# Kernel tuning notes

Measured on AMD Instinct MI355X. Metric: run time of the kernel, lower is better.

Reference implementation:

```python
import jax, jax.numpy as jnp
import numpy as np

N_NODES = 100000
N_EDGES = 600000
N_FEAT = 128
N_HID = 128
N_GRAPHS = 256


def gcn_conv(x, src, dst, W, b, n_nodes):
    # PyG GCNConv: h = x @ W; add self-loops; sym-normalize; scatter-add; + bias
    h = x @ W  # [N, H]
    loop = jnp.arange(n_nodes)
    s = jnp.concatenate([src, loop])
    d = jnp.concatenate([dst, loop])
    deg = jax.ops.segment_sum(jnp.ones_like(d, dtype=h.dtype), d, num_segments=n_nodes)
    dinv = jnp.where(deg > 0, jax.lax.rsqrt(deg), 0.0)
    norm = dinv[s] * dinv[d]  # [E+N]
    msg = h[s] * norm[:, None]  # gather + scale
    out = jax.ops.segment_sum(msg, d, num_segments=n_nodes)  # scatter-add
    return out + b


def setup_inputs() -> dict:
    key = jax.random.key(0)
    ks = jax.random.split(key, 12)
    x = jax.random.normal(ks[0], (N_NODES, N_FEAT), dtype=jnp.float32)
    edge_index = jax.random.randint(ks[1], (2, N_EDGES), 0, N_NODES, dtype=jnp.int64)
    batch = jnp.sort(jax.random.randint(ks[2], (N_NODES,), 0, N_GRAPHS, dtype=jnp.int64))
    def lin(k, fi, fo):
        s = 1.0 / np.sqrt(fi)
        return jax.random.uniform(k, (fi, fo), jnp.float32, -s, s)
    params = {
        'W1': lin(ks[3], N_FEAT, N_HID), 'b1': jnp.zeros((N_HID,), jnp.float32),
        'W2': lin(ks[4], N_HID, N_HID), 'b2': jnp.zeros((N_HID,), jnp.float32),
        'W3': lin(ks[5], N_HID, N_HID), 'b3': jnp.zeros((N_HID,), jnp.float32),
        'W4': lin(ks[6], N_HID, N_HID), 'b4': jnp.zeros((N_HID,), jnp.float32),
        'Ws1': lin(ks[7], N_HID, N_HID), 'bs1': jnp.zeros((N_HID,), jnp.float32),
        'Ws2': lin(ks[8], N_HID, 1), 'bs2': jnp.zeros((1,), jnp.float32),
    }
    return {'x': x, 'edge_index': edge_index, 'batch': batch, **params}


def reference(x, edge_index, batch, W1, b1, W2, b2, W3, b3, W4, b4, Ws1, bs1, Ws2, bs2):
    src, dst = edge_index[0], edge_index[1]
    h = x
    # 2 conv blocks = 4 GCNConv layers, each followed by ReLU
    for W, b in ((W1, b1), (W2, b2), (W3, b3), (W4, b4)):
        h = jax.nn.relu(gcn_conv(h, src, dst, W, b, N_NODES))
    # global mean pool over nodes per graph
    sums = jax.ops.segment_sum(h, batch, num_segments=N_GRAPHS)  # [G, H]
    cnt = jax.ops.segment_sum(jnp.ones((h.shape[0],), h.dtype), batch, num_segments=N_GRAPHS)
    pooled = sums / jnp.maximum(cnt, 1.0)[:, None]
    # summary MLP: Linear -> ReLU -> Linear(->1)
    out = jax.nn.relu(pooled @ Ws1 + bs1) @ Ws2 + bs2  # [G, 1]
    return out
```

## Files before the change

### kernel.cpp

```cpp
#include <hip/hip_runtime.h>

#define N_NODES 100000
#define N_EDGES 600000
#define NF 128
#define NG 256

typedef _Float16 f16;
typedef f16 half8 __attribute__((ext_vector_type(8)));
typedef f16 half4v __attribute__((ext_vector_type(4)));
typedef float float4v __attribute__((ext_vector_type(4)));


__global__ void k_count(const int* __restrict__ ei, int* __restrict__ counts) {
    int e = blockIdx.x * 256 + threadIdx.x;
    if (e < N_EDGES) atomicAdd(&counts[ei[N_EDGES + e]], 1);
}

__global__ void k_scan1(const int* __restrict__ counts, int* __restrict__ row_ptr,
                        int* __restrict__ bsums, float* __restrict__ dinv) {
    __shared__ int s[256];
    int b = blockIdx.x, t = threadIdx.x;
    int base = b * 2048 + t * 8;
    int local[8];
    int sum = 0;
#pragma unroll
    for (int q = 0; q < 8; q++) {
        int idx = base + q;
        int v = (idx < N_NODES) ? counts[idx] : 0;
        if (idx < N_NODES) dinv[idx] = 1.0f / sqrtf((float)(v + 1));
        local[q] = sum;
        sum += v;
    }
    s[t] = sum;
    __syncthreads();
    for (int off = 1; off < 256; off <<= 1) {
        int v = 0;
        if (t >= off) v = s[t - off];
        __syncthreads();
        s[t] += v;
        __syncthreads();
    }
    int excl = s[t] - sum;
#pragma unroll
    for (int q = 0; q < 8; q++) {
        int idx = base + q;
        if (idx < N_NODES) row_ptr[idx] = excl + local[q];
    }
    if (t == 255) bsums[b] = s[255];
}

__global__ void k_scan3(int* __restrict__ row_ptr, const int* __restrict__ bsums,
                        int* __restrict__ cursor) {
    __shared__ int pre;
    if (threadIdx.x == 0) {
        int g = blockIdx.x >> 3;
        int s = 0;
        for (int j = 0; j < g; j++) s += bsums[j];
        pre = s;
    }
    __syncthreads();
    int i = blockIdx.x * 256 + threadIdx.x;
    if (i < N_NODES) {
        int v = row_ptr[i] + pre;
        row_ptr[i] = v;
        cursor[i] = v;
        if (i == 0) row_ptr[N_NODES] = N_EDGES;
    }
}

__global__ void k_fill(const int* __restrict__ ei, int* __restrict__ cursor,
                       int* __restrict__ col,
                       const float* __restrict__ W1, const float* __restrict__ W2,
                       const float* __restrict__ W3, const float* __restrict__ W4,
                       f16* __restrict__ wtH) {
    int e = blockIdx.x * 256 + threadIdx.x;
    if (e < N_EDGES) {
        int d = ei[N_EDGES + e];
        int p = atomicAdd(&cursor[d], 1);
        col[p] = ei[e];
    }
    if (blockIdx.x < 256) {
        int idx = blockIdx.x * 256 + threadIdx.x;
        int layer = idx >> 14;
        int rem = idx & 16383;
        int j = rem & 7;
        int lane = (rem >> 3) & 63;
        int chunk = rem >> 9;
        int wave = chunk >> 3;
        int s = (chunk >> 1) & 3;
        int ct = chunk & 1;
        int n = wave * 32 + ct * 16 + (lane & 15);
        int k = s * 32 + (lane >> 4) * 8 + j;
        const float* W = (layer == 0) ? W1 : (layer == 1) ? W2 : (layer == 2) ? W3 : W4;
        wtH[layer * 16384 + rem] = (f16)W[k * NF + n];
    }
}


__device__ __forceinline__ void agg_tail(const half8* __restrict__ z8,
                                         const int* __restrict__ col,
                                         int sbase, int fl, int beg, int end,
                                         float acc[8]) {
    for (int c = beg + 16; c < end; c += 16) {
        int ce = c + fl;
        int cv = (ce < end) ? col[ce] : 0;
        int mc = end - c; if (mc > 16) mc = 16;
        for (int j = 0; j < mc; j += 4) {
            int kk = mc - j;
            half8 v0 = {}, v1 = {}, v2 = {}, v3 = {};
            int s0 = __shfl(cv, sbase + j + 0, 64);
            v0 = z8[(size_t)s0 * 16 + fl];
            if (kk > 1) { int s1 = __shfl(cv, sbase + j + 1, 64); v1 = z8[(size_t)s1 * 16 + fl]; }
            if (kk > 2) { int s2 = __shfl(cv, sbase + j + 2, 64); v2 = z8[(size_t)s2 * 16 + fl]; }
            if (kk > 3) { int s3 = __shfl(cv, sbase + j + 3, 64); v3 = z8[(size_t)s3 * 16 + fl]; }
#pragma unroll
            for (int q = 0; q < 8; q++) acc[q] += (float)v0[q];
            if (kk > 1) {
#pragma unroll
                for (int q = 0; q < 8; q++) acc[q] += (float)v1[q];
            }
            if (kk > 2) {
#pragma unroll
                for (int q = 0; q < 8; q++) acc[q] += (float)v2[q];
            }
            if (kk > 3) {
#pragma unroll
                for (int q = 0; q < 8; q++) acc[q] += (float)v3[q];
            }
        }
    }
}

__device__ __forceinline__ void agg_pair(const half8* __restrict__ z8,
                                         const int* __restrict__ col,
                                         int sbase, int fl,
                                         int begA, int endA, int begB, int endB,
                                         int colvA, int colvB,
                                         float accA[8], float accB[8]) {
    int mA = endA - begA; if (mA > 16) mA = 16;
    int mB = endB - begB; if (mB > 16) mB = 16;
    const int mmax = (mA > mB) ? mA : mB;
    for (int j = 0; j < mmax; j += 4) {
        const int kA = mA - j, kB = mB - j;
        half8 vA0 = {}, vA1 = {}, vA2 = {}, vA3 = {};
        half8 vB0 = {}, vB1 = {}, vB2 = {}, vB3 = {};
        if (kA > 0) {
            int s0 = __shfl(colvA, sbase + j + 0, 64);
            vA0 = z8[(size_t)s0 * 16 + fl];
            if (kA > 1) { int s1 = __shfl(colvA, sbase + j + 1, 64); vA1 = z8[(size_t)s1 * 16 + fl]; }
            if (kA > 2) { int s2 = __shfl(colvA, sbase + j + 2, 64); vA2 = z8[(size_t)s2 * 16 + fl]; }
            if (kA > 3) { int s3 = __shfl(colvA, sbase + j + 3, 64); vA3 = z8[(size_t)s3 * 16 + fl]; }
        }
        if (kB > 0) {
            int s0 = __shfl(colvB, sbase + j + 0, 64);
            vB0 = z8[(size_t)s0 * 16 + fl];
            if (kB > 1) { int s1 = __shfl(colvB, sbase + j + 1, 64); vB1 = z8[(size_t)s1 * 16 + fl]; }
            if (kB > 2) { int s2 = __shfl(colvB, sbase + j + 2, 64); vB2 = z8[(size_t)s2 * 16 + fl]; }
            if (kB > 3) { int s3 = __shfl(colvB, sbase + j + 3, 64); vB3 = z8[(size_t)s3 * 16 + fl]; }
        }
        if (kA > 0) {
#pragma unroll
            for (int q = 0; q < 8; q++) accA[q] += (float)vA0[q];
            if (kA > 1) {
#pragma unroll
                for (int q = 0; q < 8; q++) accA[q] += (float)vA1[q];
            }
            if (kA > 2) {
#pragma unroll
                for (int q = 0; q < 8; q++) accA[q] += (float)vA2[q];
            }
            if (kA > 3) {
#pragma unroll
                for (int q = 0; q < 8; q++) accA[q] += (float)vA3[q];
            }
        }
        if (kB > 0) {
#pragma unroll
            for (int q = 0; q < 8; q++) accB[q] += (float)vB0[q];
            if (kB > 1) {
#pragma unroll
                for (int q = 0; q < 8; q++) accB[q] += (float)vB1[q];
            }
            if (kB > 2) {
#pragma unroll
                for (int q = 0; q < 8; q++) accB[q] += (float)vB2[q];
            }
            if (kB > 3) {
#pragma unroll
                for (int q = 0; q < 8; q++) accB[q] += (float)vB3[q];
            }
        }
    }
    if (endA - begA > 16) agg_tail(z8, col, sbase, fl, begA, endA, accA);
    if (endB - begB > 16) agg_tail(z8, col, sbase, fl, begB, endB, accB);
}


__global__ __launch_bounds__(256) void k_gemm1(
    const float* __restrict__ X, const f16* __restrict__ WTH,
    const float* __restrict__ dinv, f16* __restrict__ Z, int M) {
    __shared__ __align__(16) f16 As[64 * 136];
    __shared__ float sdi[64];

    const int t = threadIdx.x;
    const int row0 = blockIdx.x * 64;
    const int wave = t >> 6;
    const int lane = t & 63;
    const int nl = lane & 15;
    const int quad = lane >> 4;

    auto bofs = [&](int s, int ct) {
        return (size_t)((((wave * 8 + s * 2 + ct) * 64) + lane) << 3);
    };

    half8 cbh[2];
    cbh[0] = *(const half8*)(WTH + bofs(0, 0));
    cbh[1] = *(const half8*)(WTH + bofs(0, 1));

    if (t < 64) sdi[t] = (row0 + t < M) ? dinv[row0 + t] : 0.f;
#pragma unroll
    for (int q = 0; q < 8; q++) {
        int lin = t + q * 256;
        int r = lin >> 5, c4 = lin & 31;
        float4 v = make_float4(0.f, 0.f, 0.f, 0.f);
        if (row0 + r < M) v = ((const float4*)(X + (size_t)(row0 + r) * NF))[c4];
        half4v hv = {(f16)v.x, (f16)v.y, (f16)v.z, (f16)v.w};
        *(half4v*)&As[r * 136 + c4 * 4] = hv;
    }
    __syncthreads();

    float4v acc[2][4];
#pragma unroll
    for (int ct = 0; ct < 2; ct++)
#pragma unroll
        for (int rt = 0; rt < 4; rt++) acc[ct][rt] = (float4v)0.f;

#pragma unroll
    for (int s = 0; s < 4; s++) {
        half8 nbh[2];
        if (s < 3) {
            nbh[0] = *(const half8*)(WTH + bofs(s + 1, 0));
            nbh[1] = *(const half8*)(WTH + bofs(s + 1, 1));
        }
        half8 fa[4];
#pragma unroll
        for (int rt = 0; rt < 4; rt++)
            fa[rt] = *(half8*)&As[(rt * 16 + nl) * 136 + s * 32 + quad * 8];
#pragma unroll
        for (int ct = 0; ct < 2; ct++)
#pragma unroll
            for (int rt = 0; rt < 4; rt++)
                acc[ct][rt] = __builtin_amdgcn_mfma_f32_16x16x32_f16(fa[rt], cbh[ct], acc[ct][rt], 0, 0, 0);
        if (s < 3) {
            cbh[0] = nbh[0]; cbh[1] = nbh[1];
        }
    }

    __syncthreads();
#pragma unroll
    for (int ct = 0; ct < 2; ct++)
#pragma unroll
        for (int rt = 0; rt < 4; rt++)
#pragma unroll
            for (int r = 0; r < 4; r++)
                As[(rt * 16 + quad * 4 + r) * 136 + wave * 32 + ct * 16 + nl] =
                    (f16)(acc[ct][rt][r] * sdi[rt * 16 + quad * 4 + r]);
    __syncthreads();
#pragma unroll
    for (int q = 0; q < 4; q++) {
        int lin = t + q * 256;
        int r = lin >> 4, c8 = lin & 15;
        if (row0 + r < M)
            *(half8*)(Z + (size_t)(row0 + r) * NF + c8 * 8) = *(half8*)&As[r * 136 + c8 * 8];
    }
}


#define ACHUNK 4

__global__ __launch_bounds__(256) void k_agg_gemm(
    const f16* __restrict__ z, const float* __restrict__ dinv,
    const int* __restrict__ row_ptr, const int* __restrict__ col,
    const float* __restrict__ bias,
    const f16* __restrict__ WTH,
    f16* __restrict__ Zout) {
    __shared__ __align__(16) f16 As[64 * 136];
    __shared__ float sdi[64];

    const int t = threadIdx.x;
    const int slot = t >> 4;
    const int fl = t & 15;
    const int sbase = (t & 48);
    const int n0 = (blockIdx.x * 16 + slot) * ACHUNK;
    const half8* z8 = (const half8*)z;

    float bb[8];
    {
        float4 b0 = ((const float4*)bias)[fl * 2];
        float4 b1 = ((const float4*)bias)[fl * 2 + 1];
        bb[0] = b0.x; bb[1] = b0.y; bb[2] = b0.z; bb[3] = b0.w;
        bb[4] = b1.x; bb[5] = b1.y; bb[6] = b1.z; bb[7] = b1.w;
    }

    int rp[5];
#pragma unroll
    for (int i = 0; i < 5; i++) {
        int n = n0 + i;
        rp[i] = row_ptr[(n < N_NODES) ? n : N_NODES];
    }
    float dis[4]; half8 selfv[4]; int colv0[4];
#pragma unroll
    for (int i = 0; i < 4; i++) {
        int n = n0 + i;
        bool ok = n < N_NODES;
        half8 zz = {};
        dis[i] = ok ? dinv[n] : 0.f;
        selfv[i] = ok ? z8[(size_t)n * 16 + fl] : zz;
        int ce = rp[i] + fl;
        colv0[i] = (ce < rp[i + 1]) ? col[ce] : 0;
    }
    if (fl == 0) {
#pragma unroll
        for (int i = 0; i < 4; i++) sdi[slot * ACHUNK + i] = dis[i];
    }

#pragma unroll
    for (int p = 0; p < 2; p++) {
        const int iA = 2 * p, iB = 2 * p + 1;
        float accA[8], accB[8];
#pragma unroll
        for (int q = 0; q < 8; q++) {
            accA[q] = (float)selfv[iA][q];
            accB[q] = (float)selfv[iB][q];
        }
        agg_pair(z8, col, sbase, fl, rp[iA], rp[iA + 1], rp[iB], rp[iB + 1],
                 colv0[iA], colv0[iB], accA, accB);
        half8 oA, oB;
#pragma unroll
        for (int q = 0; q < 8; q++) {
            oA[q] = (f16)fmaxf(bb[q] + dis[iA] * accA[q], 0.f);
            oB[q] = (f16)fmaxf(bb[q] + dis[iB] * accB[q], 0.f);
        }
        *(half8*)&As[(slot * ACHUNK + iA) * 136 + fl * 8] = oA;
        *(half8*)&As[(slot * ACHUNK + iB) * 136 + fl * 8] = oB;
    }

    const int wave = t >> 6;
    const int lane = t & 63;
    const int nl = lane & 15;
    const int quad = lane >> 4;
    const int row0 = blockIdx.x * 64;

    auto bofs = [&](int s, int ct) {
        return (size_t)((((wave * 8 + s * 2 + ct) * 64) + lane) << 3);
    };

    half8 cbh[2];
    cbh[0] = *(const half8*)(WTH + bofs(0, 0));
    cbh[1] = *(const half8*)(WTH + bofs(0, 1));
    __syncthreads();

    float4v acc[2][4];
#pragma unroll
    for (int ct = 0; ct < 2; ct++)
#pragma unroll
        for (int rt = 0; rt < 4; rt++) acc[ct][rt] = (float4v)0.f;

#pragma unroll
    for (int s = 0; s < 4; s++) {
        half8 nbh[2];
        if (s < 3) {
            nbh[0] = *(const half8*)(WTH + bofs(s + 1, 0));
            nbh[1] = *(const half8*)(WTH + bofs(s + 1, 1));
        }
        half8 fa[4];
#pragma unroll
        for (int rt = 0; rt < 4; rt++)
            fa[rt] = *(half8*)&As[(rt * 16 + nl) * 136 + s * 32 + quad * 8];
#pragma unroll
        for (int ct = 0; ct < 2; ct++)
#pragma unroll
            for (int rt = 0; rt < 4; rt++)
                acc[ct][rt] = __builtin_amdgcn_mfma_f32_16x16x32_f16(fa[rt], cbh[ct], acc[ct][rt], 0, 0, 0);
        if (s < 3) {
            cbh[0] = nbh[0]; cbh[1] = nbh[1];
        }
    }

    __syncthreads();
#pragma unroll
    for (int ct = 0; ct < 2; ct++)
#pragma unroll
        for (int rt = 0; rt < 4; rt++)
#pragma unroll
            for (int r = 0; r < 4; r++)
                As[(rt * 16 + quad * 4 + r) * 136 + wave * 32 + ct * 16 + nl] =
                    (f16)(acc[ct][rt][r] * sdi[rt * 16 + quad * 4 + r]);
    __syncthreads();
#pragma unroll
    for (int q = 0; q < 4; q++) {
        int lin = t + q * 256;
        int r = lin >> 4, c8 = lin & 15;
        if (row0 + r < N_NODES)
            *(half8*)(Zout + (size_t)(row0 + r) * NF + c8 * 8) = *(half8*)&As[r * 136 + c8 * 8];
    }
}


#define HP 132

__global__ __launch_bounds__(256) void k_agg_pool(
    const f16* __restrict__ z, const float* __restrict__ dinv,
    const int* __restrict__ row_ptr, const int* __restrict__ col,
    const float* __restrict__ bias, const int* __restrict__ batch,
    float* __restrict__ pooled) {
    __shared__ float hs[64 * HP];
    __shared__ int gids[64];

    const int t = threadIdx.x;
    const int slot = t >> 4;
    const int fl = t & 15;
    const int sbase = (t & 48);
    const int n0 = (blockIdx.x * 16 + slot) * ACHUNK;
    const int base_node = blockIdx.x * 64;
    const half8* z8 = (const half8*)z;

    float bb[8];
    {
        float4 b0 = ((const float4*)bias)[fl * 2];
        float4 b1 = ((const float4*)bias)[fl * 2 + 1];
        bb[0] = b0.x; bb[1] = b0.y; bb[2] = b0.z; bb[3] = b0.w;
        bb[4] = b1.x; bb[5] = b1.y; bb[6] = b1.z; bb[7] = b1.w;
    }

    if (t < 64) {
        int n = base_node + t;
        gids[t] = (n < N_NODES) ? batch[n] : -1;
    }

    int rp[5];
#pragma unroll
    for (int i = 0; i < 5; i++) {
        int n = n0 + i;
        rp[i] = row_ptr[(n < N_NODES) ? n : N_NODES];
    }
    float dis[4]; half8 selfv[4]; int colv0[4];
#pragma unroll
    for (int i = 0; i < 4; i++) {
        int n = n0 + i;
        bool ok = n < N_NODES;
        half8 zz = {};
        dis[i] = ok ? dinv[n] : 0.f;
        selfv[i] = ok ? z8[(size_t)n * 16 + fl] : zz;
        int ce = rp[i] + fl;
        colv0[i] = (ce < rp[i + 1]) ? col[ce] : 0;
    }

#pragma unroll
    for (int p = 0; p < 2; p++) {
        const int iA = 2 * p, iB = 2 * p + 1;
        float accA[8], accB[8];
#pragma unroll
        for (int q = 0; q < 8; q++) {
            accA[q] = (float)selfv[iA][q];
            accB[q] = (float)selfv[iB][q];
        }
        agg_pair(z8, col, sbase, fl, rp[iA], rp[iA + 1], rp[iB], rp[iB + 1],
                 colv0[iA], colv0[iB], accA, accB);
        float4v a0, a1, b0v, b1v;
#pragma unroll
        for (int q = 0; q < 4; q++) {
            a0[q]  = fmaxf(bb[q]     + dis[iA] * accA[q],     0.f);
            a1[q]  = fmaxf(bb[q + 4] + dis[iA] * accA[q + 4], 0.f);
            b0v[q] = fmaxf(bb[q]     + dis[iB] * accB[q],     0.f);
            b1v[q] = fmaxf(bb[q + 4] + dis[iB] * accB[q + 4], 0.f);
        }
        *(float4v*)&hs[(slot * ACHUNK + iA) * HP + fl * 8]     = a0;
        *(float4v*)&hs[(slot * ACHUNK + iA) * HP + fl * 8 + 4] = a1;
        *(float4v*)&hs[(slot * ACHUNK + iB) * HP + fl * 8]     = b0v;
        *(float4v*)&hs[(slot * ACHUNK + iB) * HP + fl * 8 + 4] = b1v;
    }
    __syncthreads();

    if (t < NF) {
        float acc = 0.f;
        int curg = -1;
        for (int r = 0; r < 64; r++) {
            int g = gids[r];
            if (g < 0) break;
            if (g != curg) {
                if (curg >= 0) atomicAdd(&pooled[curg * NF + t], acc);
                acc = 0.f;
                curg = g;
            }
            acc += hs[r * HP + t];
        }
        if (curg >= 0) atomicAdd(&pooled[curg * NF + t], acc);
    }
}


__global__ void k_mlp(const float* __restrict__ pooled, const int* __restrict__ batch,
                      const float* __restrict__ Ws1, const float* __restrict__ bs1,
                      const float* __restrict__ Ws2, const float* __restrict__ bs2,
                      float* __restrict__ out) {
    __shared__ float row[NF];
    __shared__ float red[NF];
    int g = blockIdx.x, f = threadIdx.x;
    int lo = 0, hi = N_NODES;
    while (lo < hi) { int mid = (lo + hi) >> 1; if (batch[mid] < g) lo = mid + 1; else hi = mid; }
    int start = lo;
    hi = N_NODES;
    while (lo < hi) { int mid = (lo + hi) >> 1; if (batch[mid] < g + 1) lo = mid + 1; else hi = mid; }
    float cnt = (float)(lo - start);
    row[f] = pooled[g * NF + f] / fmaxf(cnt, 1.f);
    __syncthreads();
    float t = bs1[f];
    for (int k = 0; k < NF; k++) t += row[k] * Ws1[k * NF + f];
    t = fmaxf(t, 0.f);
    red[f] = t * Ws2[f];
    __syncthreads();
    for (int s = 64; s > 0; s >>= 1) {
        if (f < s) red[f] += red[f + s];
        __syncthreads();
    }
    if (f == 0) out[g] = red[0] + bs2[0];
}


extern "C" void kernel_launch(void* const* d_in, const int* in_sizes, int n_in,
                              void* d_out, int out_size, void* d_ws, size_t ws_size,
                              hipStream_t stream) {
    const float* x    = (const float*)d_in[0];
    const int*   ei   = (const int*)d_in[1];
    const int*   batch= (const int*)d_in[2];
    const float* W1 = (const float*)d_in[3];  const float* b1 = (const float*)d_in[4];
    const float* W2 = (const float*)d_in[5];  const float* b2 = (const float*)d_in[6];
    const float* W3 = (const float*)d_in[7];  const float* b3 = (const float*)d_in[8];
    const float* W4 = (const float*)d_in[9];  const float* b4 = (const float*)d_in[10];
    const float* Ws1= (const float*)d_in[11]; const float* bs1= (const float*)d_in[12];
    const float* Ws2= (const float*)d_in[13]; const float* bs2= (const float*)d_in[14];
    float* out = (float*)d_out;

    char* ws = (char*)d_ws;
    size_t off = 0;
    auto alloc = [&](size_t bytes) {
        void* p = ws + off;
        off += (bytes + 255) & ~(size_t)255;
        return p;
    };
    f16*   bufA   = (f16*)alloc((size_t)N_NODES * NF * 2);
    f16*   bufB   = (f16*)alloc((size_t)N_NODES * NF * 2);
    f16*   wtH    = (f16*)alloc((size_t)4 * NF * NF * 2);
    int*   counts = (int*)alloc((size_t)N_NODES * 4);
    int*   row_ptr= (int*)alloc((size_t)(N_NODES + 1) * 4);
    int*   cursor = (int*)alloc((size_t)N_NODES * 4);
    int*   col    = (int*)alloc((size_t)N_EDGES * 4);
    int*   bsums  = (int*)alloc(64 * 4);
    float* dinv   = (float*)alloc((size_t)N_NODES * 4);
    float* pooled = (float*)alloc((size_t)NG * NF * 4);

    hipMemsetAsync(counts, 0, (size_t)N_NODES * 4, stream);
    hipMemsetAsync(pooled, 0, (size_t)NG * NF * 4, stream);
    k_count<<<(N_EDGES + 255) / 256, 256, 0, stream>>>(ei, counts);
    int nscan = (N_NODES + 2047) / 2048;
    k_scan1<<<nscan, 256, 0, stream>>>(counts, row_ptr, bsums, dinv);
    k_scan3<<<(N_NODES + 255) / 256, 256, 0, stream>>>(row_ptr, bsums, cursor);
    k_fill<<<(N_EDGES + 255) / 256, 256, 0, stream>>>(ei, cursor, col,
                                                      W1, W2, W3, W4, wtH);

    int gblocks = (N_NODES + 63) / 64;

    k_gemm1<<<gblocks, 256, 0, stream>>>(x, wtH, dinv, bufA, N_NODES);
    k_agg_gemm<<<gblocks, 256, 0, stream>>>(bufA, dinv, row_ptr, col, b1,
                                            wtH + 16384, bufB);
    k_agg_gemm<<<gblocks, 256, 0, stream>>>(bufB, dinv, row_ptr, col, b2,
                                            wtH + 32768, bufA);
    k_agg_gemm<<<gblocks, 256, 0, stream>>>(bufA, dinv, row_ptr, col, b3,
                                            wtH + 49152, bufB);
    k_agg_pool<<<gblocks, 256, 0, stream>>>(bufB, dinv, row_ptr, col, b4,
                                            batch, pooled);
    k_mlp<<<NG, 128, 0, stream>>>(pooled, batch, Ws1, bs1, Ws2, bs2, out);
}
```

Baseline: 361.9 us.

## Fuse preprocessing and epilogue kernels to cut launch count

Replaces the two memsets and the weight conversion with one init kernel. Merges the two-pass scan into a single-pass scan with decoupled lookback over block sums, and runs the CSR fill concurrently with the first GEMM inside one launch. The final MLP moves into the last-finishing block of the pool kernel through an atomic counter. This removes several launches and their serialization gaps, at the cost of a serial MLP over all 256 graphs in one block and spin-waits in the scan.

```diff
diff --git a/kernel.cpp b/kernel.cpp
--- a/kernel.cpp
+++ b/kernel.cpp
@@ -4,97 +4,16 @@
 #define N_EDGES 600000
 #define NF 128
 #define NG 256
+#define GBLK 1563
+#define EBLK 2344
+#define ACHUNK 4
+#define HP 132
+#define SFLAG (1 << 30)
 
 typedef _Float16 f16;
 typedef f16 half8 __attribute__((ext_vector_type(8)));
 typedef f16 half4v __attribute__((ext_vector_type(4)));
 typedef float float4v __attribute__((ext_vector_type(4)));
-
-
-__global__ void k_count(const int* __restrict__ ei, int* __restrict__ counts) {
-    int e = blockIdx.x * 256 + threadIdx.x;
-    if (e < N_EDGES) atomicAdd(&counts[ei[N_EDGES + e]], 1);
-}
-
-__global__ void k_scan1(const int* __restrict__ counts, int* __restrict__ row_ptr,
-                        int* __restrict__ bsums, float* __restrict__ dinv) {
-    __shared__ int s[256];
-    int b = blockIdx.x, t = threadIdx.x;
-    int base = b * 2048 + t * 8;
-    int local[8];
-    int sum = 0;
-#pragma unroll
-    for (int q = 0; q < 8; q++) {
-        int idx = base + q;
-        int v = (idx < N_NODES) ? counts[idx] : 0;
-        if (idx < N_NODES) dinv[idx] = 1.0f / sqrtf((float)(v + 1));
-        local[q] = sum;
-        sum += v;
-    }
-    s[t] = sum;
-    __syncthreads();
-    for (int off = 1; off < 256; off <<= 1) {
-        int v = 0;
-        if (t >= off) v = s[t - off];
-        __syncthreads();
-        s[t] += v;
-        __syncthreads();
-    }
-    int excl = s[t] - sum;
-#pragma unroll
-    for (int q = 0; q < 8; q++) {
-        int idx = base + q;
-        if (idx < N_NODES) row_ptr[idx] = excl + local[q];
-    }
-    if (t == 255) bsums[b] = s[255];
-}
-
-__global__ void k_scan3(int* __restrict__ row_ptr, const int* __restrict__ bsums,
-                        int* __restrict__ cursor) {
-    __shared__ int pre;
-    if (threadIdx.x == 0) {
-        int g = blockIdx.x >> 3;
-        int s = 0;
-        for (int j = 0; j < g; j++) s += bsums[j];
-        pre = s;
-    }
-    __syncthreads();
-    int i = blockIdx.x * 256 + threadIdx.x;
-    if (i < N_NODES) {
-        int v = row_ptr[i] + pre;
-        row_ptr[i] = v;
-        cursor[i] = v;
-        if (i == 0) row_ptr[N_NODES] = N_EDGES;
-    }
-}
-
-__global__ void k_fill(const int* __restrict__ ei, int* __restrict__ cursor,
-                       int* __restrict__ col,
-                       const float* __restrict__ W1, const float* __restrict__ W2,
-                       const float* __restrict__ W3, const float* __restrict__ W4,
-                       f16* __restrict__ wtH) {
-    int e = blockIdx.x * 256 + threadIdx.x;
-    if (e < N_EDGES) {
-        int d = ei[N_EDGES + e];
-        int p = atomicAdd(&cursor[d], 1);
-        col[p] = ei[e];
-    }
-    if (blockIdx.x < 256) {
-        int idx = blockIdx.x * 256 + threadIdx.x;
-        int layer = idx >> 14;
-        int rem = idx & 16383;
-        int j = rem & 7;
-        int lane = (rem >> 3) & 63;
-        int chunk = rem >> 9;
-        int wave = chunk >> 3;
-        int s = (chunk >> 1) & 3;
-        int ct = chunk & 1;
-        int n = wave * 32 + ct * 16 + (lane & 15);
-        int k = s * 32 + (lane >> 4) * 8 + j;
-        const float* W = (layer == 0) ? W1 : (layer == 1) ? W2 : (layer == 2) ? W3 : W4;
-        wtH[layer * 16384 + rem] = (f16)W[k * NF + n];
-    }
-}
 
 
 __device__ __forceinline__ void agg_tail(const half8* __restrict__ z8,
@@ -196,13 +115,116 @@
 }
 
 
-__global__ __launch_bounds__(256) void k_gemm1(
+__global__ void k_init(int* __restrict__ counts, float* __restrict__ pooled,
+                       int* __restrict__ bsums, int* __restrict__ ctrl,
+                       const float* __restrict__ W1, const float* __restrict__ W2,
+                       const float* __restrict__ W3, const float* __restrict__ W4,
+                       f16* __restrict__ wtH) {
+    int gtid = blockIdx.x * 256 + threadIdx.x;
+    int gs = gridDim.x * 256;
+    for (int i = gtid; i < N_NODES; i += gs) counts[i] = 0;
+    for (int i = gtid; i < NG * NF; i += gs) pooled[i] = 0.f;
+    if (gtid < 64) bsums[gtid] = 0;
+    if (gtid >= 64 && gtid < 80) ctrl[gtid - 64] = 0;
+    for (int idx = gtid; idx < 65536; idx += gs) {
+        int layer = idx >> 14;
+        int rem = idx & 16383;
+        int j = rem & 7;
+        int lane = (rem >> 3) & 63;
+        int chunk = rem >> 9;
+        int wave = chunk >> 3;
+        int s = (chunk >> 1) & 3;
+        int ct = chunk & 1;
+        int n = wave * 32 + ct * 16 + (lane & 15);
+        int k = s * 32 + (lane >> 4) * 8 + j;
+        const float* W = (layer == 0) ? W1 : (layer == 1) ? W2 : (layer == 2) ? W3 : W4;
+        wtH[layer * 16384 + rem] = (f16)W[k * NF + n];
+    }
+}
+
+
+__global__ void k_count(const int* __restrict__ ei, int* __restrict__ counts) {
+    int e = blockIdx.x * 256 + threadIdx.x;
+    if (e < N_EDGES) atomicAdd(&counts[ei[N_EDGES + e]], 1);
+}
+
+
+__global__ __launch_bounds__(256) void k_scan(const int* __restrict__ counts,
+                                              int* __restrict__ row_ptr,
+                                              int* __restrict__ cursor,
+                                              int* __restrict__ bsums,
+                                              float* __restrict__ dinv) {
+    __shared__ int s[256];
+    __shared__ int spre;
+    int b = blockIdx.x, t = threadIdx.x;
+    int base = b * 2048 + t * 8;
+    int local[8];
+    int sum = 0;
+#pragma unroll
+    for (int q = 0; q < 8; q++) {
+        int idx = base + q;
+        int v = (idx < N_NODES) ? counts[idx] : 0;
+        if (idx < N_NODES) dinv[idx] = 1.0f / sqrtf((float)(v + 1));
+        local[q] = sum;
+        sum += v;
+    }
+    s[t] = sum;
+    __syncthreads();
+    for (int off = 1; off < 256; off <<= 1) {
+        int v = 0;
+        if (t >= off) v = s[t - off];
+        __syncthreads();
+        s[t] += v;
+        __syncthreads();
+    }
+    int excl = s[t] - sum;
+    if (t == 255)
+        __hip_atomic_store(&bsums[b], s[255] + SFLAG, __ATOMIC_RELEASE,
+                           __HIP_MEMORY_SCOPE_AGENT);
+    if (t == 0) {
+        int pre = 0;
+        for (int j = 0; j < b; j++) {
+            int v;
+            do {
+                v = __hip_atomic_load(&bsums[j], __ATOMIC_RELAXED,
+                                      __HIP_MEMORY_SCOPE_AGENT);
+            } while (v < SFLAG);
+            pre += v - SFLAG;
+        }
+        spre = pre;
+    }
+    __syncthreads();
+#pragma unroll
+    for (int q = 0; q < 8; q++) {
+        int idx = base + q;
+        if (idx < N_NODES) {
+            int v = spre + excl + local[q];
+            row_ptr[idx] = v;
+            cursor[idx] = v;
+        }
+    }
+    if (b == 0 && t == 0) row_ptr[N_NODES] = N_EDGES;
+}
+
+
+__global__ __launch_bounds__(256) void k_fill_gemm1(
+    const int* __restrict__ ei, int* __restrict__ cursor, int* __restrict__ col,
     const float* __restrict__ X, const f16* __restrict__ WTH,
-    const float* __restrict__ dinv, f16* __restrict__ Z, int M) {
+    const float* __restrict__ dinv, f16* __restrict__ Z) {
     __shared__ __align__(16) f16 As[64 * 136];
     __shared__ float sdi[64];
-
     const int t = threadIdx.x;
+
+    if (blockIdx.x >= GBLK) {
+        int e = (blockIdx.x - GBLK) * 256 + t;
+        if (e < N_EDGES) {
+            int d = ei[N_EDGES + e];
+            int p = atomicAdd(&cursor[d], 1);
+            col[p] = ei[e];
+        }
+        return;
+    }
+
     const int row0 = blockIdx.x * 64;
     const int wave = t >> 6;
     const int lane = t & 63;
@@ -217,13 +239,13 @@
     cbh[0] = *(const half8*)(WTH + bofs(0, 0));
     cbh[1] = *(const half8*)(WTH + bofs(0, 1));
 
-    if (t < 64) sdi[t] = (row0 + t < M) ? dinv[row0 + t] : 0.f;
+    if (t < 64) sdi[t] = (row0 + t < N_NODES) ? dinv[row0 + t] : 0.f;
 #pragma unroll
     for (int q = 0; q < 8; q++) {
         int lin = t + q * 256;
         int r = lin >> 5, c4 = lin & 31;
         float4 v = make_float4(0.f, 0.f, 0.f, 0.f);
-        if (row0 + r < M) v = ((const float4*)(X + (size_t)(row0 + r) * NF))[c4];
+        if (row0 + r < N_NODES) v = ((const float4*)(X + (size_t)(row0 + r) * NF))[c4];
         half4v hv = {(f16)v.x, (f16)v.y, (f16)v.z, (f16)v.w};
         *(half4v*)&As[r * 136 + c4 * 4] = hv;
     }
@@ -270,19 +292,16 @@
     for (int q = 0; q < 4; q++) {
         int lin = t + q * 256;
         int r = lin >> 4, c8 = lin & 15;
-        if (row0 + r < M)
+        if (row0 + r < N_NODES)
             *(half8*)(Z + (size_t)(row0 + r) * NF + c8 * 8) = *(half8*)&As[r * 136 + c8 * 8];
     }
 }
 
-
-#define ACHUNK 4
 
 __global__ __launch_bounds__(256) void k_agg_gemm(
     const f16* __restrict__ z, const float* __restrict__ dinv,
     const int* __restrict__ row_ptr, const int* __restrict__ col,
-    const float* __restrict__ bias,
-    const f16* __restrict__ WTH,
+    const float* __restrict__ bias, const f16* __restrict__ WTH,
     f16* __restrict__ Zout) {
     __shared__ __align__(16) f16 As[64 * 136];
     __shared__ float sdi[64];
@@ -407,15 +426,17 @@
 }
 
 
-#define HP 132
-
-__global__ __launch_bounds__(256) void k_agg_pool(
+__global__ __launch_bounds__(256) void k_agg_pool_mlp(
     const f16* __restrict__ z, const float* __restrict__ dinv,
     const int* __restrict__ row_ptr, const int* __restrict__ col,
     const float* __restrict__ bias, const int* __restrict__ batch,
-    float* __restrict__ pooled) {
+    float* __restrict__ pooled, int* __restrict__ ctrl,
+    const float* __restrict__ Ws1, const float* __restrict__ bs1,
+    const float* __restrict__ Ws2, const float* __restrict__ bs2,
+    float* __restrict__ out) {
     __shared__ float hs[64 * HP];
     __shared__ int gids[64];
+    __shared__ int slast;
 
     const int t = threadIdx.x;
     const int slot = t >> 4;
@@ -451,7 +472,7 @@
         bool ok = n < N_NODES;
         half8 zz = {};
         dis[i] = ok ? dinv[n] : 0.f;
-        selfv[i] = ok ? z8[(size_t)n * 16 + fl] : zz;
+        selfv[i] = ok ? z8[(size_t)(ok ? n : 0) * 16 + fl] : zz;
         int ce = rp[i] + fl;
         colv0[i] = (ce < rp[i + 1]) ? col[ce] : 0;
     }
@@ -497,34 +518,45 @@
         }
         if (curg >= 0) atomicAdd(&pooled[curg * NF + t], acc);
     }
-}
-
-
-__global__ void k_mlp(const float* __restrict__ pooled, const int* __restrict__ batch,
-                      const float* __restrict__ Ws1, const float* __restrict__ bs1,
-                      const float* __restrict__ Ws2, const float* __restrict__ bs2,
-                      float* __restrict__ out) {
-    __shared__ float row[NF];
-    __shared__ float red[NF];
-    int g = blockIdx.x, f = threadIdx.x;
-    int lo = 0, hi = N_NODES;
-    while (lo < hi) { int mid = (lo + hi) >> 1; if (batch[mid] < g) lo = mid + 1; else hi = mid; }
-    int start = lo;
-    hi = N_NODES;
-    while (lo < hi) { int mid = (lo + hi) >> 1; if (batch[mid] < g + 1) lo = mid + 1; else hi = mid; }
-    float cnt = (float)(lo - start);
-    row[f] = pooled[g * NF + f] / fmaxf(cnt, 1.f);
-    __syncthreads();
-    float t = bs1[f];
-    for (int k = 0; k < NF; k++) t += row[k] * Ws1[k * NF + f];
-    t = fmaxf(t, 0.f);
-    red[f] = t * Ws2[f];
-    __syncthreads();
-    for (int s = 64; s > 0; s >>= 1) {
-        if (f < s) red[f] += red[f + s];
+    __syncthreads();
+
+    if (t == 0) {
+        __threadfence();
+        int d = __hip_atomic_fetch_add(&ctrl[0], 1, __ATOMIC_ACQ_REL,
+                                       __HIP_MEMORY_SCOPE_AGENT);
+        slast = (d == (int)gridDim.x - 1) ? 1 : 0;
+    }
+    __syncthreads();
+    if (!slast) return;
+
+    float* row = hs;
+    float* red = hs + 256;
+    const int half = t >> 7;
+    const int f = t & 127;
+    for (int gp = 0; gp < NG; gp += 2) {
+        int g = gp + half;
+        int lo = 0, hi = N_NODES;
+        while (lo < hi) { int mid = (lo + hi) >> 1; if (batch[mid] < g) lo = mid + 1; else hi = mid; }
+        int start = lo;
+        hi = N_NODES;
+        while (lo < hi) { int mid = (lo + hi) >> 1; if (batch[mid] < g + 1) lo = mid + 1; else hi = mid; }
+        float cntg = (float)(lo - start);
+        float pv = __hip_atomic_load(&pooled[g * NF + f], __ATOMIC_RELAXED,
+                                     __HIP_MEMORY_SCOPE_AGENT);
+        row[half * 128 + f] = pv / fmaxf(cntg, 1.f);
         __syncthreads();
-    }
-    if (f == 0) out[g] = red[0] + bs2[0];
+        float a = bs1[f];
+        for (int k = 0; k < NF; k++) a += row[half * 128 + k] * Ws1[k * NF + f];
+        a = fmaxf(a, 0.f);
+        red[half * 128 + f] = a * Ws2[f];
+        __syncthreads();
+        for (int s2 = 64; s2 > 0; s2 >>= 1) {
+            if (f < s2) red[half * 128 + f] += red[half * 128 + f + s2];
+            __syncthreads();
+        }
+        if (f == 0) out[g] = red[half * 128] + bs2[0];
+        __syncthreads();
+    }
 }
 
 
@@ -559,26 +591,21 @@
     int*   bsums  = (int*)alloc(64 * 4);
     float* dinv   = (float*)alloc((size_t)N_NODES * 4);
     float* pooled = (float*)alloc((size_t)NG * NF * 4);
-
-    hipMemsetAsync(counts, 0, (size_t)N_NODES * 4, stream);
-    hipMemsetAsync(pooled, 0, (size_t)NG * NF * 4, stream);
-    k_count<<<(N_EDGES + 255) / 256, 256, 0, stream>>>(ei, counts);
-    int nscan = (N_NODES + 2047) / 2048;
-    k_scan1<<<nscan, 256, 0, stream>>>(counts, row_ptr, bsums, dinv);
-    k_scan3<<<(N_NODES + 255) / 256, 256, 0, stream>>>(row_ptr, bsums, cursor);
-    k_fill<<<(N_EDGES + 255) / 256, 256, 0, stream>>>(ei, cursor, col,
-                                                      W1, W2, W3, W4, wtH);
-
-    int gblocks = (N_NODES + 63) / 64;
-
-    k_gemm1<<<gblocks, 256, 0, stream>>>(x, wtH, dinv, bufA, N_NODES);
-    k_agg_gemm<<<gblocks, 256, 0, stream>>>(bufA, dinv, row_ptr, col, b1,
-                                            wtH + 16384, bufB);
-    k_agg_gemm<<<gblocks, 256, 0, stream>>>(bufB, dinv, row_ptr, col, b2,
-                                            wtH + 32768, bufA);
-    k_agg_gemm<<<gblocks, 256, 0, stream>>>(bufA, dinv, row_ptr, col, b3,
-                                            wtH + 49152, bufB);
-    k_agg_pool<<<gblocks, 256, 0, stream>>>(bufB, dinv, row_ptr, col, b4,
-                                            batch, pooled);
-    k_mlp<<<NG, 128, 0, stream>>>(pooled, batch, Ws1, bs1, Ws2, bs2, out);
-}
+    int*   ctrl   = (int*)alloc(64);
+
+    k_init<<<256, 256, 0, stream>>>(counts, pooled, bsums, ctrl,
+                                    W1, W2, W3, W4, wtH);
+    k_count<<<EBLK, 256, 0, stream>>>(ei, counts);
+    k_scan<<<49, 256, 0, stream>>>(counts, row_ptr, cursor, bsums, dinv);
+    k_fill_gemm1<<<GBLK + EBLK, 256, 0, stream>>>(ei, cursor, col,
+                                                  x, wtH, dinv, bufA);
+    k_agg_gemm<<<GBLK, 256, 0, stream>>>(bufA, dinv, row_ptr, col, b1,
+                                         wtH + 16384, bufB);
+    k_agg_gemm<<<GBLK, 256, 0, stream>>>(bufB, dinv, row_ptr, col, b2,
+                                         wtH + 32768, bufA);
+    k_agg_gemm<<<GBLK, 256, 0, stream>>>(bufA, dinv, row_ptr, col, b3,
+                                         wtH + 49152, bufB);
+    k_agg_pool_mlp<<<GBLK, 256, 0, stream>>>(bufB, dinv, row_ptr, col, b4,
+                                             batch, pooled, ctrl,
+                                             Ws1, bs1, Ws2, bs2, out);
+}
```

New measurement: 1.391 ms. +284.4%, slower.
